# Kernel tuning notes

Measured on AMD Instinct MI355X. Metric: run time of the kernel, lower is better.

The kernel has to match this reference:

```python
import jax, jax.numpy as jnp
import numpy as np

N_NODES = 50000
N_EDGES = 800000
IN_CH = 128
HID = 48
HEADS = 2
HH = HID * HEADS  # 96
N_GRAPHS = 64
NEG_SLOPE = 0.2


def _gat_layer(x, src, dst, n, W, a_src, a_dst, b, heads, out_ch):
    # x: [N, in]; W: [in, heads*out]; a_src/a_dst: [heads, out]; b: [heads*out]
    h = (x @ W).reshape(n, heads, out_ch)              # [N, H, C]
    es = (h * a_src).sum(-1)                            # [N, H]
    ed = (h * a_dst).sum(-1)                            # [N, H]
    e = jax.nn.leaky_relu(es[src] + ed[dst], NEG_SLOPE)  # [E, H]
    m = jax.ops.segment_max(e, dst, num_segments=n)      # segment softmax (stable)
    p = jnp.exp(e - m[dst])
    denom = jax.ops.segment_sum(p, dst, num_segments=n)
    alpha = p / denom[dst]                               # [E, H]
    out = jax.ops.segment_sum(alpha[:, :, None] * h[src], dst, num_segments=n)
    return out.reshape(n, heads * out_ch) + b


def setup_inputs() -> dict:
    key = jax.random.key(0)
    ks = jax.random.split(key, 20)
    x = jax.random.normal(ks[0], (N_NODES, IN_CH), dtype=jnp.float32)
    edge_index = jax.random.randint(ks[1], (2, N_EDGES), 0, N_NODES, dtype=jnp.int64)
    edge_weight = jax.random.uniform(ks[2], (N_EDGES,), dtype=jnp.float32)
    batch = jnp.sort(jax.random.randint(ks[3], (N_NODES,), 0, N_GRAPHS, dtype=jnp.int64))
    s = 0.1
    params = {
        'W1': jax.random.normal(ks[4], (IN_CH, HH)) * s,
        'as1': jax.random.normal(ks[5], (HEADS, HID)) * s,
        'ad1': jax.random.normal(ks[6], (HEADS, HID)) * s,
        'b1': jnp.zeros((HH,), jnp.float32),
        'W2': jax.random.normal(ks[7], (HH, HH)) * s,
        'as2': jax.random.normal(ks[8], (1, HH)) * s,
        'ad2': jax.random.normal(ks[9], (1, HH)) * s,
        'b2': jnp.zeros((HH,), jnp.float32),
        'W3': jax.random.normal(ks[10], (HH, HH)) * s,
        'as3': jax.random.normal(ks[11], (1, HH)) * s,
        'ad3': jax.random.normal(ks[12], (1, HH)) * s,
        'b3': jnp.zeros((HH,), jnp.float32),
        'W4': jax.random.normal(ks[13], (HH, HH)) * s,
        'as4': jax.random.normal(ks[14], (1, HH)) * s,
        'ad4': jax.random.normal(ks[15], (1, HH)) * s,
        'b4': jnp.zeros((HH,), jnp.float32),
        'Wc': jax.random.normal(ks[16], (HH, 1)) * s,
        'bc': jnp.zeros((1,), jnp.float32),
    }
    return {'x': x, 'edge_index': edge_index, 'edge_weight': edge_weight,
            'batch': batch, **params}


def reference(x, edge_index, edge_weight, batch,
              W1, as1, ad1, b1, W2, as2, ad2, b2,
              W3, as3, ad3, b3, W4, as4, ad4, b4, Wc, bc):
    n = x.shape[0]
    loops = jnp.arange(n, dtype=edge_index.dtype)  # PyG GATConv add_self_loops=True
    src = jnp.concatenate([edge_index[0], loops])
    dst = jnp.concatenate([edge_index[1], loops])
    # edge_weight is ignored by GATConv when edge_dim=None (faithful to PyG)
    h = jax.nn.relu(_gat_layer(x, src, dst, n, W1, as1, ad1, b1, HEADS, HID))
    h = jax.nn.relu(_gat_layer(h, src, dst, n, W2, as2, ad2, b2, 1, HH))
    h = jax.nn.relu(_gat_layer(h, src, dst, n, W3, as3, ad3, b3, 1, HH))
    h = jax.nn.relu(_gat_layer(h, src, dst, n, W4, as4, ad4, b4, 1, HH))
    # global_mean_pool
    sums = jax.ops.segment_sum(h, batch, num_segments=N_GRAPHS)
    cnts = jax.ops.segment_sum(jnp.ones((n, 1), h.dtype), batch, num_segments=N_GRAPHS)
    pooled = sums / jnp.maximum(cnts, 1.0)
    return jax.nn.sigmoid(pooled @ Wc + bc)
```

## Files before the change

### kernel.cpp

```cpp
#include <hip/hip_runtime.h>
#include <hip/hip_bf16.h>

#define NN 50000
#define NE 800000
#define NG 64
#define NBUCK 256
#define BN 196
#define EPB 4096
#define HB 196
#define SMAX 4200

typedef __attribute__((ext_vector_type(8))) short short8;
typedef __attribute__((ext_vector_type(4))) float float4v;
typedef __attribute__((ext_vector_type(2))) float float2v;

__device__ __forceinline__ float bf2f(unsigned short u){
    unsigned v = ((unsigned)u) << 16; float f; __builtin_memcpy(&f, &v, 4); return f;
}
__device__ __forceinline__ unsigned short f2bf(float f){
    unsigned u; __builtin_memcpy(&u, &f, 4);
    u = (u + 0x7fffu + ((u >> 16) & 1u)) >> 16;
    return (unsigned short)u;
}
__device__ __forceinline__ float lrelu(float v){ return v > 0.f ? v : 0.2f * v; }

__device__ __forceinline__ float ldflex(const void* p, long i, int isbf){
    if (isbf) return bf2f(((const unsigned short*)p)[i]);
    return ((const float*)p)[i];
}
__device__ __forceinline__ int ldidx(const int* p, long i, int is64){
    return p[is64 ? (i << 1) : i];
}

__device__ __forceinline__ unsigned pk_bf16(float a, float b){
    unsigned r;
    asm("v_cvt_pk_bf16_f32 %0, %1, %2" : "=v"(r) : "v"(a), "v"(b));
    return r;
}

__device__ __forceinline__ unsigned int enc_fp8_1(float f){
    unsigned u; __builtin_memcpy(&u, &f, 4);
    unsigned s = (u >> 24) & 0x80u;
    float a = fabsf(f); a = fminf(a, 448.f);
    float x = a * 0x1p-120f;
    unsigned xu; __builtin_memcpy(&xu, &x, 4);
    unsigned r = (xu + 0x7FFFFu + ((xu >> 20) & 1u)) >> 20;
    if (r > 0x7Eu) r = 0x7Eu;
    return s | r;
}
__device__ __forceinline__ unsigned short pk_fp8(float a, float b){
#if __has_builtin(__builtin_amdgcn_cvt_pk_fp8_f32)
    int r = __builtin_amdgcn_cvt_pk_fp8_f32(a, b, 0, false);
    return (unsigned short)(r & 0xFFFF);
#else
    return (unsigned short)(enc_fp8_1(a) | (enc_fp8_1(b) << 8));
#endif
}
__device__ __forceinline__ float dec_fp8_manual(unsigned int byte){
    unsigned bits = ((byte & 0x80u) << 24) | ((byte & 0x7Fu) << 20);
    float f; __builtin_memcpy(&f, &bits, 4);
    return f * 0x1p120f;
}
__device__ __forceinline__ void dec_fp8x4_pk(unsigned int v, float2v& lo, float2v& hi){
#if __has_builtin(__builtin_amdgcn_cvt_pk_f32_fp8)
    lo = __builtin_amdgcn_cvt_pk_f32_fp8((int)v, false);
    hi = __builtin_amdgcn_cvt_pk_f32_fp8((int)v, true);
#else
    lo[0] = dec_fp8_manual(v & 0xFF);
    lo[1] = dec_fp8_manual((v >> 8) & 0xFF);
    hi[0] = dec_fp8_manual((v >> 16) & 0xFF);
    hi[1] = dec_fp8_manual((v >> 24) & 0xFF);
#endif
}

__device__ __forceinline__ int detect_isbf_local(const unsigned short* xu){
    int hit = 0;
    for (int i = 0; i < 128; i++){
        int ex = (xu[2 * i] >> 7) & 0xFF;
        if (ex >= 100 && ex <= 140) hit++;
    }
    return (hit >= 64) ? 1 : 0;
}
__device__ __forceinline__ int detect_i64_local(const unsigned int* u){
    int z = 0;
    for (int i = 0; i < 128; i++) if (u[2 * i + 1] == 0) z++;
    return (z >= 120) ? 1 : 0;
}

__global__ __launch_bounds__(256) void prep_kernel(const unsigned short* __restrict__ xu,
                                                   const unsigned int* __restrict__ eiu,
                                                   const unsigned int* __restrict__ bu,
                                                   const void* W0, const void* W1,
                                                   const void* W2, const void* W3,
                                                   unsigned short* __restrict__ wt_all,
                                                   const int* __restrict__ ei,
                                                   int* __restrict__ hist,
                                                   int* __restrict__ flags,
                                                   float* __restrict__ pooled,
                                                   int* __restrict__ gcnt){
    int b = blockIdx.x, tid = threadIdx.x;
    if (b == 0){
        for (int i = tid; i < NG * 96; i += 256) pooled[i] = 0.f;
        if (tid < NG) gcnt[tid] = 0;
        if (tid == 0){
            flags[0] = detect_isbf_local(xu);
            flags[1] = detect_i64_local(eiu);
            int z = 0;
            for (int i = 0; i < 128; i++) if (bu[49745 + 2 * i] == 0) z++;
            flags[2] = (z >= 120) ? 1 : 0;
        }
        return;
    }
    if (b <= 4){
        __shared__ int lf;
        if (tid == 0) lf = detect_isbf_local(xu);
        __syncthreads();
        int isbf = lf;
        int l = b - 1;
        const void* W = (l == 0) ? W0 : (l == 1) ? W1 : (l == 2) ? W2 : W3;
        int K = (l == 0) ? 128 : 96;
        unsigned short* out = wt_all + ((l == 0) ? 0 : (96 * 128 + (l - 1) * 96 * 96));
        int tot = 96 * K;
        for (int i = tid; i < tot; i += 256){
            int c = i / K, k = i - c * K;
            out[i] = f2bf(ldflex(W, (long)k * 96 + c, isbf));
        }
        return;
    }
    __shared__ int h[NBUCK];
    __shared__ int lf2;
    if (tid == 0) lf2 = detect_i64_local(eiu);
    h[tid] = 0;
    __syncthreads();
    int f64 = lf2;
    int hb = b - 5;
    long e0 = (long)hb * EPB + tid;
    #pragma unroll
    for (int r = 0; r < 16; r++){
        long e = e0 + r * 256;
        if (e < NE){
            int d = ldidx(ei, NE + e, f64);
            atomicAdd(&h[d / BN], 1);
        }
    }
    __syncthreads();
    hist[(long)hb * NBUCK + tid] = h[tid];
}

__global__ __launch_bounds__(256) void bscatter_kernel(const int* __restrict__ ei,
                                                       const int* __restrict__ hist,
                                                       int* __restrict__ bucketBase,
                                                       int2* __restrict__ ebuf){
    __shared__ int h[NBUCK], lofs[NBUCK], gbase[NBUCK], lcur[NBUCK], bb[NBUCK];
    __shared__ int2 lstage[EPB];
    __shared__ int lf;
    int tid = threadIdx.x;
    int myb = blockIdx.x;
    if (tid == 0) lf = detect_i64_local((const unsigned int*)ei);
    __syncthreads();
    int f64 = lf;
    int pre = 0, tot = 0;
    for (int b2 = 0; b2 < HB; b2++){
        int v = hist[b2 * NBUCK + tid];
        tot += v;
        if (b2 < myb) pre += v;
    }
    bb[tid] = tot; __syncthreads();
    for (int off = 1; off < 256; off <<= 1){
        int x = bb[tid];
        int y = (tid >= off) ? bb[tid - off] : 0;
        __syncthreads();
        bb[tid] = x + y;
        __syncthreads();
    }
    int bucket0 = bb[tid] - tot;
    if (myb == 0){
        bucketBase[tid] = bucket0;
        if (tid == 255) bucketBase[256] = bb[255];
    }
    gbase[tid] = bucket0 + pre;
    h[tid] = 0;
    __syncthreads();
    int2 ed[16]; int bk[16];
    long e0 = (long)myb * EPB + tid;
    #pragma unroll
    for (int r = 0; r < 16; r++){
        long e = e0 + r * 256;
        if (e < NE){
            int s = ldidx(ei, e, f64);
            int d = ldidx(ei, NE + e, f64);
            ed[r] = make_int2(s, d);
            bk[r] = d / BN;
            atomicAdd(&h[bk[r]], 1);
        } else bk[r] = -1;
    }
    __syncthreads();
    int v = h[tid];
    lofs[tid] = v; __syncthreads();
    for (int off = 1; off < 256; off <<= 1){
        int x = lofs[tid];
        int y = (tid >= off) ? lofs[tid - off] : 0;
        __syncthreads();
        lofs[tid] = x + y;
        __syncthreads();
    }
    int excl = lofs[tid] - v;
    lofs[tid] = excl;
    lcur[tid] = excl;
    __syncthreads();
    #pragma unroll
    for (int r = 0; r < 16; r++){
        if (bk[r] >= 0){
            int p = atomicAdd(&lcur[bk[r]], 1);
            lstage[p] = ed[r];
        }
    }
    __syncthreads();
    long base = (long)myb * EPB;
    int cnt = (NE - base < EPB) ? (int)(NE - base) : EPB;
    for (int j = tid; j < cnt; j += 256){
        int2 e = lstage[j];
        int i = e.y / BN;
        ebuf[gbase[i] + j - lofs[i]] = e;
    }
}

__global__ __launch_bounds__(256) void place_kernel(const int2* __restrict__ ebuf,
                                                    const int* __restrict__ bucketBase,
                                                    int* __restrict__ row_ptr,
                                                    int* __restrict__ csr){
    __shared__ int nh[BN];
    __shared__ int nofs[256];
    __shared__ int lcur[BN];
    __shared__ int stage[SMAX];
    int k = blockIdx.x, tid = threadIdx.x;
    int n0 = k * BN;
    int seg0 = bucketBase[k];
    int len = bucketBase[k + 1] - seg0;
    for (int i = tid; i < BN; i += 256) nh[i] = 0;
    __syncthreads();
    for (int j = tid; j < len; j += 256){
        int2 e = ebuf[seg0 + j];
        atomicAdd(&nh[e.y - n0], 1);
    }
    __syncthreads();
    int v = (tid < BN) ? nh[tid] : 0;
    nofs[tid] = v; __syncthreads();
    for (int off = 1; off < 256; off <<= 1){
        int x = nofs[tid];
        int y = (tid >= off) ? nofs[tid - off] : 0;
        __syncthreads();
        nofs[tid] = x + y;
        __syncthreads();
    }
    int excl = nofs[tid] - v;
    if (tid < BN){
        lcur[tid] = excl;
        int node = n0 + tid;
        if (node < NN) row_ptr[node] = seg0 + excl;
    }
    if (k == NBUCK - 1 && tid == 0) row_ptr[NN] = NE;
    __syncthreads();
    if (len <= SMAX){
        for (int j = tid; j < len; j += 256){
            int2 e = ebuf[seg0 + j];
            int p = atomicAdd(&lcur[e.y - n0], 1);
            stage[p] = e.x;
        }
        __syncthreads();
        for (int j = tid; j < len; j += 256)
            csr[seg0 + j] = stage[j];
    } else {
        for (int j = tid; j < len; j += 256){
            int2 e = ebuf[seg0 + j];
            int p = atomicAdd(&lcur[e.y - n0], 1);
            csr[seg0 + p] = e.x;
        }
    }
}

template<int K, int H, bool L1>
__global__ __launch_bounds__(256) void gemm_mfma(const void* __restrict__ Ain,
                                                 const unsigned short* __restrict__ Wt,
                                                 const void* __restrict__ as_,
                                                 const void* __restrict__ ad_,
                                                 unsigned short* __restrict__ hq16,
                                                 float* __restrict__ es,
                                                 float* __restrict__ ed,
                                                 float* __restrict__ pself,
                                                 const int* __restrict__ flags){
    __shared__ union {
        struct { unsigned short xs[64 * 40]; unsigned short wt[96 * 40]; } s;
        float hs[64 * 104];
    } u;
    __shared__ float2 aa[96];
    int tid = threadIdx.x;
    int row0 = blockIdx.x * 64;
    int lane = tid & 63, w = tid >> 6;
    int m = lane & 15, q = lane >> 4;
    int isbf = flags[0];
    if (tid < 96)
        aa[tid] = make_float2(ldflex(as_, tid, isbf), ldflex(ad_, tid, isbf));
    float4v acc[6];
    #pragma unroll
    for (int ct = 0; ct < 6; ct++) acc[ct] = (float4v){0.f, 0.f, 0.f, 0.f};

    int sr = tid >> 2, kp = tid & 3;
    int rr = row0 + sr; if (rr >= NN) rr = NN - 1;

    for (int k0 = 0; k0 < K; k0 += 32){
        uint4 av;
        if (L1 && !isbf){
            const float* xf = (const float*)Ain + (size_t)rr * K + k0 + kp * 8;
            float4 f1 = *(const float4*)xf;
            float4 f2 = *(const float4*)(xf + 4);
            av.x = pk_bf16(f1.x, f1.y);
            av.y = pk_bf16(f1.z, f1.w);
            av.z = pk_bf16(f2.x, f2.y);
            av.w = pk_bf16(f2.z, f2.w);
        } else {
            av = *(const uint4*)((const unsigned short*)Ain + (size_t)rr * K + k0 + kp * 8);
        }
        *(uint4*)(u.s.xs + sr * 40 + kp * 8) = av;
        for (int i = tid; i < 96 * 4; i += 256){
            int c = i >> 2, kq = i & 3;
            *(uint4*)(u.s.wt + c * 40 + kq * 8) =
                *(const uint4*)(Wt + (size_t)c * K + k0 + kq * 8);
        }
        __syncthreads();
        short8 a = *(const short8*)(u.s.xs + (w * 16 + m) * 40 + q * 8);
        #pragma unroll
        for (int ct = 0; ct < 6; ct++){
            short8 b = *(const short8*)(u.s.wt + (ct * 16 + m) * 40 + q * 8);
            acc[ct] = __builtin_amdgcn_mfma_f32_16x16x32_bf16(a, b, acc[ct], 0, 0, 0);
        }
        __syncthreads();
    }

    #pragma unroll
    for (int ct = 0; ct < 6; ct++)
        #pragma unroll
        for (int r = 0; r < 4; r++)
            u.hs[(w * 16 + q * 4 + r) * 104 + ct * 16 + m] = acc[ct][r];
    __syncthreads();

    int rl = tid >> 2, part = tid & 3;
    int row = row0 + rl;
    float hv[24];
    #pragma unroll
    for (int jj = 0; jj < 6; jj++)
        *(float4v*)&hv[jj * 4] = *(const float4v*)&u.hs[rl * 104 + part * 24 + jj * 4];

    float pes = 0.f, ped = 0.f;
    #pragma unroll
    for (int i = 0; i < 24; i++){
        float2 wv = aa[part * 24 + i];
        pes += hv[i] * wv.x;
        ped += hv[i] * wv.y;
    }
    pes += __shfl_xor(pes, 1); ped += __shfl_xor(ped, 1);
    if (H == 1){ pes += __shfl_xor(pes, 2); ped += __shfl_xor(ped, 2); }

    if (row < NN){
        if (part == 0){
            es[(long)row * H] = pes; ed[(long)row * H] = ped;
            pself[(long)row * H] = __expf(lrelu(pes + ped));
        }
        if (H == 2 && part == 2){
            es[(long)row * H + 1] = pes; ed[(long)row * H + 1] = ped;
            pself[(long)row * H + 1] = __expf(lrelu(pes + ped));
        }
        unsigned short wds[12];
        #pragma unroll
        for (int j = 0; j < 12; j++) wds[j] = pk_fp8(hv[2 * j], hv[2 * j + 1]);
        uint2* dst = (uint2*)hq16 + (long)row * 16 + part * 3;
        #pragma unroll
        for (int j2 = 0; j2 < 3; j2++){
            uint2 v;
            v.x = (unsigned)wds[4 * j2] | ((unsigned)wds[4 * j2 + 1] << 16);
            v.y = (unsigned)wds[4 * j2 + 2] | ((unsigned)wds[4 * j2 + 3] << 16);
            dst[j2] = v;
        }
    }
}

template<int H>
__global__ __launch_bounds__(256) void attn_kernel(const unsigned int* __restrict__ hq,
                                                   const float* __restrict__ es,
                                                   const float* __restrict__ ed,
                                                   const float* __restrict__ pself,
                                                   const int* __restrict__ row_ptr,
                                                   const int* __restrict__ csr,
                                                   const void* __restrict__ bias,
                                                   unsigned int* __restrict__ outb,
                                                   const int* __restrict__ flags){
    int lane = threadIdx.x & 63;
    int d = blockIdx.x * 4 + (threadIdx.x >> 6);
    if (d >= NN) return;
    int isbf = flags[0];
    int beg = row_ptr[d], deg = row_ptr[d + 1] - beg;
    int g = lane & 3;
    int c12 = lane >> 2;
    int head = (H == 2) ? ((c12 >= 6) ? 1 : 0) : 0;
    int m = lane - 48;
    float edd0 = ed[(long)d * H];
    float edd1 = (H == 2) ? ed[(long)d * H + 1] : edd0;

    int s_nxt = 0; float p0_nxt = 0.f, p1_nxt = 0.f;
    if (lane >= 48 && m < deg){
        int s = csr[beg + m];
        s_nxt = s * 32;
        if (H == 1){
            p0_nxt = __expf(lrelu(es[s] + edd0));
        } else {
            float2 e2 = *(const float2*)&es[2 * (long)s];
            p0_nxt = __expf(lrelu(e2.x + edd0));
            p1_nxt = __expf(lrelu(e2.y + edd1));
        }
    }

    float2v acc[4];
    #pragma unroll
    for (int k = 0; k < 4; k++) acc[k] = (float2v){0.f, 0.f};
    float dnl = 0.f;
    int cq = 2 * c12;

    for (int base = 0; base < deg; base += 16){
        int s_cur = s_nxt; float p0c = p0_nxt, p1c = p1_nxt;
        int nb = base + 16;
        s_nxt = 0; p0_nxt = 0.f; p1_nxt = 0.f;
        if (lane >= 48 && nb + m < deg){
            int s = csr[beg + nb + m];
            s_nxt = s * 32;
            if (H == 1){
                p0_nxt = __expf(lrelu(es[s] + edd0));
            } else {
                float2 e2 = *(const float2*)&es[2 * (long)s];
                p0_nxt = __expf(lrelu(e2.x + edd0));
                p1_nxt = __expf(lrelu(e2.y + edd1));
            }
        }
        int cnt = deg - base; if (cnt > 16) cnt = 16;
        int steps = (cnt + 3) >> 2;
        auto do_step = [&](int t){
            int idx = 48 + 4 * t + g;
            int s32 = __shfl(s_cur, idx);
            float p;
            if (H == 2){
                float p0 = __shfl(p0c, idx);
                float p1 = __shfl(p1c, idx);
                p = head ? p1 : p0;
            } else {
                p = __shfl(p0c, idx);
            }
            uint2 v = make_uint2(0u, 0u);
            if (lane < 48) v = *(const uint2*)(hq + (unsigned)s32 + cq);
            float2v lo0, hi0, lo1, hi1;
            dec_fp8x4_pk(v.x, lo0, hi0);
            dec_fp8x4_pk(v.y, lo1, hi1);
            float2v p2 = {p, p};
            acc[0] += p2 * lo0; acc[1] += p2 * hi0;
            acc[2] += p2 * lo1; acc[3] += p2 * hi1;
            dnl += p;
        };
        if (steps == 4){
            do_step(0); do_step(1); do_step(2); do_step(3);
        } else {
            for (int t = 0; t < steps; t++) do_step(t);
        }
    }

    float t8[8];
    #pragma unroll
    for (int k = 0; k < 4; k++){ t8[2 * k] = acc[k][0]; t8[2 * k + 1] = acc[k][1]; }
    #pragma unroll
    for (int k = 0; k < 8; k++){
        t8[k] += __shfl_xor(t8[k], 1);
        t8[k] += __shfl_xor(t8[k], 2);
    }
    dnl += __shfl_xor(dnl, 1);
    dnl += __shfl_xor(dnl, 2);

    if (lane < 48 && g < 2){
        float ps = pself[(long)d * H + head];
        float rdn = 1.f / (dnl + ps);
        unsigned sv = hq[(unsigned)d * 32u + cq + g];
        float2v lo, hi;
        dec_fp8x4_pk(sv, lo, hi);
        int c0 = 4 * (cq + g);
        float o0 = (t8[4 * g + 0] + ps * lo[0]) * rdn + ldflex(bias, c0 + 0, isbf);
        float o1 = (t8[4 * g + 1] + ps * lo[1]) * rdn + ldflex(bias, c0 + 1, isbf);
        float o2 = (t8[4 * g + 2] + ps * hi[0]) * rdn + ldflex(bias, c0 + 2, isbf);
        float o3 = (t8[4 * g + 3] + ps * hi[1]) * rdn + ldflex(bias, c0 + 3, isbf);
        uint2 st;
        st.x = pk_bf16(fmaxf(o0, 0.f), fmaxf(o1, 0.f));
        st.y = pk_bf16(fmaxf(o2, 0.f), fmaxf(o3, 0.f));
        ((uint2*)outb)[(long)d * 24 + cq + g] = st;
    }
}

__global__ __launch_bounds__(64) void pool_kernel(const unsigned int* __restrict__ bufb,
                                                  const int* __restrict__ batch,
                                                  float* __restrict__ pooled,
                                                  int* __restrict__ gcnt,
                                                  const int* __restrict__ flags){
    int f64 = flags[2];
    int n0 = blockIdx.x * 32;
    if (n0 >= NN) return;
    int n1 = n0 + 32; if (n1 > NN) n1 = NN;
    int lane = threadIdx.x;
    if (lane < 48){
        float a0 = 0.f, a1 = 0.f;
        int curg = ldidx(batch, n0, f64);
        for (int nd = n0; nd < n1; nd++){
            int g = ldidx(batch, nd, f64);
            if (g != curg){
                atomicAdd(&pooled[curg * 96 + 2 * lane], a0);
                atomicAdd(&pooled[curg * 96 + 2 * lane + 1], a1);
                a0 = a1 = 0.f; curg = g;
            }
            unsigned v = bufb[(long)nd * 48 + lane];
            a0 += bf2f((unsigned short)v);
            a1 += bf2f((unsigned short)(v >> 16));
        }
        atomicAdd(&pooled[curg * 96 + 2 * lane], a0);
        atomicAdd(&pooled[curg * 96 + 2 * lane + 1], a1);
    } else if (lane == 48){
        int cnt = 0;
        int curg = ldidx(batch, n0, f64);
        for (int nd = n0; nd < n1; nd++){
            int g = ldidx(batch, nd, f64);
            if (g != curg){
                atomicAdd(&gcnt[curg], cnt);
                cnt = 0; curg = g;
            }
            cnt++;
        }
        atomicAdd(&gcnt[curg], cnt);
    }
}

__global__ void final_kernel(const float* __restrict__ pooled, const int* __restrict__ gcnt,
                             const void* __restrict__ Wc, const void* __restrict__ bc,
                             void* __restrict__ outp, const int* __restrict__ flags){
    int isbf = flags[0];
    int g = threadIdx.x;
    if (g >= NG) return;
    float cnt = (float)gcnt[g];
    if (cnt < 1.f) cnt = 1.f;
    float acc = 0.f;
    for (int c = 0; c < 96; c++)
        acc += (pooled[g * 96 + c] / cnt) * ldflex(Wc, c, isbf);
    acc += ldflex(bc, 0, isbf);
    float sg = 1.f / (1.f + __expf(-acc));
    if (isbf) ((unsigned short*)outp)[g] = f2bf(sg);
    else      ((float*)outp)[g] = sg;
}

extern "C" void kernel_launch(void* const* d_in, const int* in_sizes, int n_in,
                              void* d_out, int out_size, void* d_ws, size_t ws_size,
                              hipStream_t stream){
    const void* x     = d_in[0];
    const int* ei     = (const int*)d_in[1];
    const int* batch  = (const int*)d_in[3];
    const void* W[4]  = {d_in[4],  d_in[8],  d_in[12], d_in[16]};
    const void* AS[4] = {d_in[5],  d_in[9],  d_in[13], d_in[17]};
    const void* AD[4] = {d_in[6],  d_in[10], d_in[14], d_in[18]};
    const void* B[4]  = {d_in[7],  d_in[11], d_in[15], d_in[19]};
    const void* Wc    = d_in[20];
    const void* bc    = d_in[21];

    char* p = (char*)d_ws;
    auto alloc = [&](size_t bytes) -> void* {
        void* r = (void*)p;
        p += (bytes + 255) & ~(size_t)255;
        return r;
    };
    int* flags     = (int*)alloc(16);
    unsigned int* hq = (unsigned int*)alloc((size_t)NN * 128);
    unsigned int* buf1b = (unsigned int*)alloc((size_t)NN * 96 * 2);
    unsigned short* wt_all = (unsigned short*)alloc((size_t)(96 * 128 + 3 * 96 * 96) * 2);
    float* es      = (float*)alloc((size_t)NN * 2 * 4);
    float* ed      = (float*)alloc((size_t)NN * 2 * 4);
    float* pself   = (float*)alloc((size_t)NN * 2 * 4);
    int* row_ptr   = (int*)alloc((size_t)(NN + 1) * 4);
    int* csr       = (int*)alloc((size_t)NE * 4);
    int2* ebuf     = (int2*)alloc((size_t)NE * 8);
    int* hist      = (int*)alloc((size_t)HB * NBUCK * 4);
    int* bucketBase= (int*)alloc((size_t)(NBUCK + 1) * 4);
    float* pooled  = (float*)alloc((size_t)NG * 96 * 4);
    int* gcnt      = (int*)alloc((size_t)NG * 4);

    prep_kernel<<<5 + HB, 256, 0, stream>>>((const unsigned short*)x,
                                            (const unsigned int*)ei,
                                            (const unsigned int*)batch,
                                            W[0], W[1], W[2], W[3], wt_all,
                                            ei, hist, flags, pooled, gcnt);
    bscatter_kernel<<<HB, 256, 0, stream>>>(ei, hist, bucketBase, ebuf);
    place_kernel<<<NBUCK, 256, 0, stream>>>(ebuf, bucketBase, row_ptr, csr);

    const int GB = (NN + 63) / 64;
    const int AB = (NN + 3) / 4;
    unsigned short* wt1 = wt_all;
    unsigned short* wt2 = wt_all + 96 * 128;
    unsigned short* wt3 = wt2 + 96 * 96;
    unsigned short* wt4 = wt3 + 96 * 96;

    gemm_mfma<128, 2, true><<<GB, 256, 0, stream>>>(x, wt1, AS[0], AD[0],
                                                    (unsigned short*)hq, es, ed, pself, flags);
    attn_kernel<2><<<AB, 256, 0, stream>>>(hq, es, ed, pself, row_ptr, csr, B[0], buf1b, flags);
    unsigned short* wts[3] = {wt2, wt3, wt4};
    for (int l = 1; l < 4; l++){
        gemm_mfma<96, 1, false><<<GB, 256, 0, stream>>>(buf1b, wts[l - 1], AS[l], AD[l],
                                                        (unsigned short*)hq, es, ed, pself, flags);
        attn_kernel<1><<<AB, 256, 0, stream>>>(hq, es, ed, pself, row_ptr, csr, B[l], buf1b, flags);
    }

    pool_kernel<<<(NN + 31) / 32, 64, 0, stream>>>(buf1b, batch, pooled, gcnt, flags);
    final_kernel<<<1, 64, 0, stream>>>(pooled, gcnt, Wc, bc, d_out, flags);
}
```

Before: 398.3 us.

## Process two destination nodes per wavefront in attention kernel

The attention kernel now splits each 64-lane wavefront into two 32-lane halves, each handling its own destination node. Within a half, 24 lanes gather features (2 edges in flight per step) and 8 lanes prefetch edge metadata, replacing the old 48+16 split with 4 edges per step. This roughly halves idle lanes for the low average degree (~17), at the cost of less memory-level parallelism per node and more loop iterations. Bias loads are also vectorized into a single 4-wide load.

```diff
diff --git a/kernel.cpp b/kernel.cpp
--- a/kernel.cpp
+++ b/kernel.cpp
@@ -395,19 +395,22 @@
                                                    unsigned int* __restrict__ outb,
                                                    const int* __restrict__ flags){
     int lane = threadIdx.x & 63;
-    int d = blockIdx.x * 4 + (threadIdx.x >> 6);
+    int half = lane >> 5;
+    int l32 = lane & 31;
+    int d = blockIdx.x * 8 + ((threadIdx.x >> 6) << 1) + half;
     if (d >= NN) return;
     int isbf = flags[0];
     int beg = row_ptr[d], deg = row_ptr[d + 1] - beg;
-    int g = lane & 3;
-    int c12 = lane >> 2;
+    int g = l32 & 1;
+    int c12 = l32 >> 1;
     int head = (H == 2) ? ((c12 >= 6) ? 1 : 0) : 0;
-    int m = lane - 48;
+    int m = l32 - 24;
+    int base_meta = (half << 5) + 24;
     float edd0 = ed[(long)d * H];
     float edd1 = (H == 2) ? ed[(long)d * H + 1] : edd0;
 
     int s_nxt = 0; float p0_nxt = 0.f, p1_nxt = 0.f;
-    if (lane >= 48 && m < deg){
+    if (l32 >= 24 && m < deg){
         int s = csr[beg + m];
         s_nxt = s * 32;
         if (H == 1){
@@ -425,11 +428,11 @@
     float dnl = 0.f;
     int cq = 2 * c12;
 
-    for (int base = 0; base < deg; base += 16){
+    for (int base = 0; base < deg; base += 8){
         int s_cur = s_nxt; float p0c = p0_nxt, p1c = p1_nxt;
-        int nb = base + 16;
+        int nb = base + 8;
         s_nxt = 0; p0_nxt = 0.f; p1_nxt = 0.f;
-        if (lane >= 48 && nb + m < deg){
+        if (l32 >= 24 && nb + m < deg){
             int s = csr[beg + nb + m];
             s_nxt = s * 32;
             if (H == 1){
@@ -440,10 +443,10 @@
                 p1_nxt = __expf(lrelu(e2.y + edd1));
             }
         }
-        int cnt = deg - base; if (cnt > 16) cnt = 16;
-        int steps = (cnt + 3) >> 2;
+        int cnt = deg - base; if (cnt > 8) cnt = 8;
+        int steps = (cnt + 1) >> 1;
         auto do_step = [&](int t){
-            int idx = 48 + 4 * t + g;
+            int idx = base_meta + 2 * t + g;
             int s32 = __shfl(s_cur, idx);
             float p;
             if (H == 2){
@@ -454,7 +457,7 @@
                 p = __shfl(p0c, idx);
             }
             uint2 v = make_uint2(0u, 0u);
-            if (lane < 48) v = *(const uint2*)(hq + (unsigned)s32 + cq);
+            if (l32 < 24) v = *(const uint2*)(hq + (unsigned)s32 + cq);
             float2v lo0, hi0, lo1, hi1;
             dec_fp8x4_pk(v.x, lo0, hi0);
             dec_fp8x4_pk(v.y, lo1, hi1);
@@ -474,24 +477,30 @@
     #pragma unroll
     for (int k = 0; k < 4; k++){ t8[2 * k] = acc[k][0]; t8[2 * k + 1] = acc[k][1]; }
     #pragma unroll
-    for (int k = 0; k < 8; k++){
+    for (int k = 0; k < 8; k++)
         t8[k] += __shfl_xor(t8[k], 1);
-        t8[k] += __shfl_xor(t8[k], 2);
-    }
     dnl += __shfl_xor(dnl, 1);
-    dnl += __shfl_xor(dnl, 2);
-
-    if (lane < 48 && g < 2){
+
+    if (l32 < 24){
         float ps = pself[(long)d * H + head];
         float rdn = 1.f / (dnl + ps);
         unsigned sv = hq[(unsigned)d * 32u + cq + g];
         float2v lo, hi;
         dec_fp8x4_pk(sv, lo, hi);
         int c0 = 4 * (cq + g);
-        float o0 = (t8[4 * g + 0] + ps * lo[0]) * rdn + ldflex(bias, c0 + 0, isbf);
-        float o1 = (t8[4 * g + 1] + ps * lo[1]) * rdn + ldflex(bias, c0 + 1, isbf);
-        float o2 = (t8[4 * g + 2] + ps * hi[0]) * rdn + ldflex(bias, c0 + 2, isbf);
-        float o3 = (t8[4 * g + 3] + ps * hi[1]) * rdn + ldflex(bias, c0 + 3, isbf);
+        float b0, b1, b2, b3;
+        if (isbf){
+            const unsigned short* bp = (const unsigned short*)bias + c0;
+            ushort4 bv = *(const ushort4*)bp;
+            b0 = bf2f(bv.x); b1 = bf2f(bv.y); b2 = bf2f(bv.z); b3 = bf2f(bv.w);
+        } else {
+            float4 bv = *(const float4*)((const float*)bias + c0);
+            b0 = bv.x; b1 = bv.y; b2 = bv.z; b3 = bv.w;
+        }
+        float o0 = (t8[4 * g + 0] + ps * lo[0]) * rdn + b0;
+        float o1 = (t8[4 * g + 1] + ps * lo[1]) * rdn + b1;
+        float o2 = (t8[4 * g + 2] + ps * hi[0]) * rdn + b2;
+        float o3 = (t8[4 * g + 3] + ps * hi[1]) * rdn + b3;
         uint2 st;
         st.x = pk_bf16(fmaxf(o0, 0.f), fmaxf(o1, 0.f));
         st.y = pk_bf16(fmaxf(o2, 0.f), fmaxf(o3, 0.f));
@@ -600,7 +609,7 @@
     place_kernel<<<NBUCK, 256, 0, stream>>>(ebuf, bucketBase, row_ptr, csr);
 
     const int GB = (NN + 63) / 64;
-    const int AB = (NN + 3) / 4;
+    const int AB = (NN + 7) / 8;
     unsigned short* wt1 = wt_all;
     unsigned short* wt2 = wt_all + 96 * 128;
     unsigned short* wt3 = wt2 + 96 * 96;
```

Result: faster. 364.0 us (-8.6%).
